# Kernel tuning notes

Hardware: AMD Instinct MI355X
Metric: run time of the kernel (lower is better)

## Reference

```python
import jax, jax.numpy as jnp
import numpy as np

N, D = 8192, 512


def _l2norm(x):
    return x / jnp.linalg.norm(x, axis=-1, keepdims=True)


def setup_inputs() -> dict:
    key = jax.random.key(0)
    k1, k2 = jax.random.split(key)
    image_features = _l2norm(jax.random.normal(k1, (N, D), dtype=jnp.float32))
    text_features = _l2norm(jax.random.normal(k2, (N, D), dtype=jnp.float32))
    logit_scale = jnp.asarray(100.0, dtype=jnp.float32)  # exp(4.6), standard CLIP temperature
    return {"image_features": image_features, "text_features": text_features, "logit_scale": logit_scale}


def reference(image_features, text_features, logit_scale):
    # logits_per_image = scale * img @ txt.T ; logits_per_text is its transpose (world_size=1)
    logits = logit_scale * (image_features @ text_features.T)  # [N, N]
    n = logits.shape[0]
    idx = jnp.arange(n)
    # CE with labels = arange(N): loss = -mean(diag(log_softmax(logits)))
    lse_row = jax.nn.logsumexp(logits, axis=1)  # for logits_per_image
    lse_col = jax.nn.logsumexp(logits, axis=0)  # for logits_per_text = logits.T
    diag = logits[idx, idx]
    loss_i = jnp.mean(lse_row - diag)
    loss_t = jnp.mean(lse_col - diag)
    contrastive_loss = (loss_i + loss_t) / 2
    return contrastive_loss
```

## Files before the change

kernel.cpp:

```cpp
#include <hip/hip_runtime.h>
#include <stdint.h>

#define N_ROWS 8192
#define DDIM   512

typedef __bf16 bf16_t;
typedef bf16_t bf16x8 __attribute__((ext_vector_type(8)));
typedef float  f32x4  __attribute__((ext_vector_type(4)));

#define MFMA16 __builtin_amdgcn_mfma_f32_16x16x32_bf16

__device__ inline uint16_t f2bf(float f) {
    uint32_t u = __float_as_uint(f);
    u += 0x7FFFu + ((u >> 16) & 1u);
    return (uint16_t)(u >> 16);
}

__global__ void convert_bf16(const float* __restrict__ a, const float* __restrict__ b,
                             uint16_t* __restrict__ abf, uint16_t* __restrict__ bbf) {
    const int quads = N_ROWS * DDIM / 4;
    const int stride = gridDim.x * blockDim.x;
    for (int i = blockIdx.x * blockDim.x + threadIdx.x; i < quads; i += stride) {
        float4 va = ((const float4*)a)[i];
        float4 vb = ((const float4*)b)[i];
        ushort4 ra, rb;
        ra.x = f2bf(va.x); ra.y = f2bf(va.y); ra.z = f2bf(va.z); ra.w = f2bf(va.w);
        rb.x = f2bf(vb.x); rb.y = f2bf(vb.y); rb.z = f2bf(vb.z); rb.w = f2bf(vb.w);
        ((ushort4*)abf)[i] = ra;
        ((ushort4*)bbf)[i] = rb;
    }
}

__device__ inline void stage16(const uint8_t* g, uint8_t* lds_wave_base) {
#if __has_builtin(__builtin_amdgcn_global_load_lds)
    __builtin_amdgcn_global_load_lds(
        (const __attribute__((address_space(1))) uint32_t*)g,
        (__attribute__((address_space(3))) uint32_t*)lds_wave_base, 16, 0, 0);
#else
    *(int4*)(lds_wave_base) = *(const int4*)g;
#endif
}

__global__ void __launch_bounds__(512, 2)
clip_gemm(const uint16_t* __restrict__ A, const uint16_t* __restrict__ B,
          const float* __restrict__ scale_p,
          float* __restrict__ rowsum, float* __restrict__ colsum,
          float* __restrict__ diag) {
    __shared__ __attribute__((aligned(16))) uint8_t sh[131072];

    const int t    = threadIdx.x;
    const int wave = t >> 6;
    const int lane = t & 63;
    const int wm   = wave >> 2;
    const int wn   = wave & 3;
    const int lr   = lane & 15;
    const int lg   = lane >> 4;
    const int l7   = lane & 7;

    const int orig = blockIdx.x;
    const int xcd  = orig & 7;
    const int idx  = orig >> 3;
    const int bm   = (xcd & 3) * 8  + (idx & 7);
    const int bn   = (xcd >> 2) * 16 + (idx >> 3);

    const float s     = *scale_p;
    const float shift = s - 64.0f;

    f32x4 acc[8][4];
#pragma unroll
    for (int i = 0; i < 8; ++i)
#pragma unroll
        for (int j = 0; j < 4; ++j)
#pragma unroll
            for (int r = 0; r < 4; ++r) acc[i][j][r] = 0.0f;

    const int g16 = (((t & 7) ^ ((t >> 3) & 7)) << 4);
    const uint8_t* srcA = (const uint8_t*)A + (size_t)(bm * 256 + (t >> 3)) * 1024 + g16;
    const uint8_t* srcB = (const uint8_t*)B + (size_t)(bn * 256 + (t >> 3)) * 1024 + g16;
    uint8_t* dA = sh + wave * 1024;
    uint8_t* dB = sh + 32768 + wave * 1024;

#define STAGE8(kt, bsel) do {                                                   \
        _Pragma("unroll")                                                       \
        for (int c = 0; c < 4; ++c) {                                           \
            stage16(srcA + (size_t)(kt) * 128 + (size_t)c * 65536,              \
                    dA + (bsel) * 65536 + c * 8192);                            \
            stage16(srcB + (size_t)(kt) * 128 + (size_t)c * 65536,              \
                    dB + (bsel) * 65536 + c * 8192);                            \
        }                                                                       \
    } while (0)

    const int x0   = ((lg) ^ l7) << 4;
    const int x1   = ((4 | lg) ^ l7) << 4;
    const int aRow = (wm * 128 + lr) * 128;
    const int bRow = 32768 + (wn * 64 + lr) * 128;

    bf16x8 aC[8], bC[4], aN[8], bN[4];

#define LOAD12(AF, BF, BASE, X) do {                                            \
        const uint8_t* _b = (BASE);                                             \
        _Pragma("unroll")                                                       \
        for (int i = 0; i < 8; ++i)                                             \
            AF[i] = *(const bf16x8*)(_b + aRow + i * 2048 + (X));               \
        _Pragma("unroll")                                                       \
        for (int j = 0; j < 4; ++j)                                             \
            BF[j] = *(const bf16x8*)(_b + bRow + j * 2048 + (X));               \
    } while (0)

#define MMA32(AF, BF) do {                                                      \
        _Pragma("unroll")                                                       \
        for (int i = 0; i < 8; ++i)                                             \
            _Pragma("unroll")                                                   \
            for (int j = 0; j < 4; ++j)                                         \
                acc[i][j] = MFMA16(AF[i], BF[j], acc[i][j], 0, 0, 0);           \
    } while (0)

    STAGE8(0, 0);
    STAGE8(1, 1);
    asm volatile("s_waitcnt vmcnt(8)" ::: "memory");
    __builtin_amdgcn_s_barrier();

    LOAD12(aC, bC, sh, x0);

    for (int tt = 0; tt < 8; ++tt) {
        const uint8_t* base  = sh + (tt & 1) * 65536;
        const uint8_t* obase = sh + ((tt + 1) & 1) * 65536;

        LOAD12(aN, bN, base, x1);
        __builtin_amdgcn_s_setprio(1);
        MMA32(aC, bC);
        __builtin_amdgcn_s_setprio(0);

        asm volatile("s_waitcnt vmcnt(0)" ::: "memory");
        __builtin_amdgcn_s_barrier();

        if (tt < 6) STAGE8(tt + 2, tt & 1);
        if (tt < 7) LOAD12(aC, bC, obase, x0);
        __builtin_amdgcn_s_setprio(1);
        MMA32(aN, bN);
        __builtin_amdgcn_s_setprio(0);
    }
#undef STAGE8
#undef LOAD12
#undef MMA32

    float cp[4] = {0.f, 0.f, 0.f, 0.f};
#pragma unroll
    for (int i = 0; i < 8; ++i) {
        float rp[4] = {0.f, 0.f, 0.f, 0.f};
#pragma unroll
        for (int j = 0; j < 4; ++j) {
#pragma unroll
            for (int r = 0; r < 4; ++r) {
                const float logit = s * acc[i][j][r];
                const float e = __expf(logit - shift);
                rp[r] += e;
                cp[j] += e;
                if (bm == bn) {
                    const int rr = wm * 128 + i * 16 + lg * 4 + r;
                    const int cc = wn * 64 + j * 16 + lr;
                    if (rr == cc) diag[bm * 256 + rr] = logit;
                }
            }
        }
#pragma unroll
        for (int r = 0; r < 4; ++r) {
            float v = rp[r];
            v += __shfl_xor(v, 1);
            v += __shfl_xor(v, 2);
            v += __shfl_xor(v, 4);
            v += __shfl_xor(v, 8);
            if (lr == 0)
                atomicAdd(&rowsum[bm * 256 + wm * 128 + i * 16 + lg * 4 + r], v);
        }
    }
#pragma unroll
    for (int j = 0; j < 4; ++j) {
        float v = cp[j];
        v += __shfl_xor(v, 16);
        v += __shfl_xor(v, 32);
        if (lg == 0)
            atomicAdd(&colsum[bn * 256 + wn * 64 + j * 16 + lr], v);
    }
}

__global__ void clip_finalize(const float* __restrict__ rowsum, const float* __restrict__ colsum,
                              const float* __restrict__ diag, const float* __restrict__ scale_p,
                              float* __restrict__ out) {
    __shared__ float red[4];
    const float s = *scale_p;
    const float shift = s - 64.0f;
    const int i = blockIdx.x * 256 + threadIdx.x;
    float acc = logf(rowsum[i]) + logf(colsum[i]) + 2.f * shift - 2.f * diag[i];
#pragma unroll
    for (int m = 1; m < 64; m <<= 1) acc += __shfl_xor(acc, m);
    const int wave = threadIdx.x >> 6;
    const int lane = threadIdx.x & 63;
    if (lane == 0) red[wave] = acc;
    __syncthreads();
    if (threadIdx.x == 0) {
        atomicAdd(out, (red[0] + red[1] + red[2] + red[3]) / (2.0f * N_ROWS));
    }
}

extern "C" void kernel_launch(void* const* d_in, const int* in_sizes, int n_in,
                              void* d_out, int out_size, void* d_ws, size_t ws_size,
                              hipStream_t stream) {
    const float* img     = (const float*)d_in[0];
    const float* txt     = (const float*)d_in[1];
    const float* scale_p = (const float*)d_in[2];

    uint8_t* ws = (uint8_t*)d_ws;
    uint16_t* Abf   = (uint16_t*)ws;
    uint16_t* Bbf   = (uint16_t*)(ws + (size_t)8 * 1024 * 1024);
    float*    rowsum = (float*)(ws + (size_t)16 * 1024 * 1024);
    float*    colsum = rowsum + N_ROWS;
    float*    diag   = colsum + N_ROWS;
    float*    out    = (float*)d_out;

    hipMemsetAsync(rowsum, 0, 2 * N_ROWS * sizeof(float), stream);
    hipMemsetAsync(out, 0, sizeof(float), stream);
    convert_bf16<<<1024, 256, 0, stream>>>(img, txt, Abf, Bbf);
    clip_gemm<<<1024, 512, 0, stream>>>(Abf, Bbf, scale_p, rowsum, colsum, diag);
    clip_finalize<<<32, 256, 0, stream>>>(rowsum, colsum, diag, scale_p, out);
}
```

Baseline: 105.0 us.

## Restructure GEMM main loop into four-phase quadrant pipeline with interleaved staging

Replaces the two-half K-step loop with a per-tile schedule split into four phases. Each phase computes one 4x2 quadrant of the accumulator tile, reads the next quadrant's LDS fragments, and issues a quarter of the next tile's global-to-LDS loads. Barriers bracket each MFMA block and vmcnt gates are finer-grained, so global loads, LDS reads and MFMAs overlap more evenly instead of stalling on a full vmcnt(0) once per half step. The cost is many more barriers per tile and a more fragile register-rotation scheme.

```diff
diff --git a/kernel.cpp b/kernel.cpp
--- a/kernel.cpp
+++ b/kernel.cpp
@@ -80,69 +80,104 @@
     uint8_t* dA = sh + wave * 1024;
     uint8_t* dB = sh + 32768 + wave * 1024;
 
-#define STAGE8(kt, bsel) do {                                                   \
-        _Pragma("unroll")                                                       \
-        for (int c = 0; c < 4; ++c) {                                           \
-            stage16(srcA + (size_t)(kt) * 128 + (size_t)c * 65536,              \
-                    dA + (bsel) * 65536 + c * 8192);                            \
-            stage16(srcB + (size_t)(kt) * 128 + (size_t)c * 65536,              \
-                    dB + (bsel) * 65536 + c * 8192);                            \
-        }                                                                       \
-    } while (0)
+#define STG_A(P, BS, c) stage16((P) + (size_t)(c) * 65536, dA + (BS) * 65536 + (c) * 8192)
+#define STG_B(P, BS, c) stage16((P) + (size_t)(c) * 65536, dB + (BS) * 65536 + (c) * 8192)
 
     const int x0   = ((lg) ^ l7) << 4;
     const int x1   = ((4 | lg) ^ l7) << 4;
     const int aRow = (wm * 128 + lr) * 128;
     const int bRow = 32768 + (wn * 64 + lr) * 128;
 
-    bf16x8 aC[8], bC[4], aN[8], bN[4];
-
-#define LOAD12(AF, BF, BASE, X) do {                                            \
-        const uint8_t* _b = (BASE);                                             \
-        _Pragma("unroll")                                                       \
-        for (int i = 0; i < 8; ++i)                                             \
-            AF[i] = *(const bf16x8*)(_b + aRow + i * 2048 + (X));               \
-        _Pragma("unroll")                                                       \
-        for (int j = 0; j < 4; ++j)                                             \
-            BF[j] = *(const bf16x8*)(_b + bRow + j * 2048 + (X));               \
-    } while (0)
-
-#define MMA32(AF, BF) do {                                                      \
-        _Pragma("unroll")                                                       \
-        for (int i = 0; i < 8; ++i)                                             \
-            _Pragma("unroll")                                                   \
-            for (int j = 0; j < 4; ++j)                                         \
-                acc[i][j] = MFMA16(AF[i], BF[j], acc[i][j], 0, 0, 0);           \
-    } while (0)
-
-    STAGE8(0, 0);
-    STAGE8(1, 1);
+    bf16x8 aA[2][4], aB[2][4], aC[2][4];
+    bf16x8 bA[2][2], bB[2][2];
+
+#define RD_AH(SET, BASE, IH) do {                                              \
+        const uint8_t* _p = (const uint8_t*)(BASE) + aRow + (IH) * 8192;       \
+        _Pragma("unroll")                                                      \
+        for (int _i = 0; _i < 4; ++_i) {                                       \
+            SET[0][_i] = *(const bf16x8*)(_p + _i * 2048 + x0);                \
+            SET[1][_i] = *(const bf16x8*)(_p + _i * 2048 + x1);                \
+        }                                                                      \
+    } while (0)
+
+#define RD_BH(SET, BASE, JH) do {                                              \
+        const uint8_t* _p = (const uint8_t*)(BASE) + bRow + (JH) * 4096;       \
+        _Pragma("unroll")                                                      \
+        for (int _j = 0; _j < 2; ++_j) {                                       \
+            SET[0][_j] = *(const bf16x8*)(_p + _j * 2048 + x0);                \
+            SET[1][_j] = *(const bf16x8*)(_p + _j * 2048 + x1);                \
+        }                                                                      \
+    } while (0)
+
+#define MMQ(IH, JH, AS, BS) do {                                               \
+        _Pragma("unroll")                                                      \
+        for (int _k = 0; _k < 2; ++_k)                                         \
+        _Pragma("unroll")                                                      \
+        for (int _i = 0; _i < 4; ++_i)                                         \
+        _Pragma("unroll")                                                      \
+        for (int _j = 0; _j < 2; ++_j)                                         \
+            acc[(IH) * 4 + _i][(JH) * 2 + _j] =                                \
+                MFMA16(AS[_k][_i], BS[_k][_j],                                 \
+                       acc[(IH) * 4 + _i][(JH) * 2 + _j], 0, 0, 0);            \
+    } while (0)
+
+#define GATE_VM4  asm volatile("s_waitcnt vmcnt(4)" ::: "memory")
+#define GATE_VM0  asm volatile("s_waitcnt vmcnt(0)" ::: "memory")
+#define GATE_NONE ((void)0)
+
+#define PH(RD, STG, GATE, IH, JH, AS, BS) do {                                 \
+        RD;                                                                    \
+        STG;                                                                   \
+        GATE;                                                                  \
+        __builtin_amdgcn_s_barrier();                                          \
+        __builtin_amdgcn_s_setprio(1);                                         \
+        MMQ(IH, JH, AS, BS);                                                   \
+        __builtin_amdgcn_s_setprio(0);                                         \
+        __builtin_amdgcn_s_barrier();                                          \
+    } while (0)
+
+#define TILE(BUF, OBUF, AP, AR, PSA, PSB, BS, NEXT, GATE)                      \
+    PH(RD_AH(aC, BUF, 1),                                                      \
+       do { if (PSA) { STG_A(PSA, BS, 0); STG_A(PSA, BS, 1); } } while (0),    \
+       GATE_NONE, 0, 0, AP, bA);                                               \
+    PH(RD_BH(bB, BUF, 1),                                                      \
+       do { if (PSA) { STG_A(PSA, BS, 2); STG_A(PSA, BS, 3); } } while (0),    \
+       GATE, 1, 0, aC, bA);                                                    \
+    PH(do { if (NEXT) RD_AH(AR, OBUF, 0); } while (0),                         \
+       do { if (PSB) { STG_B(PSB, BS, 0); STG_B(PSB, BS, 1); } } while (0),    \
+       GATE_NONE, 0, 1, AP, bB);                                               \
+    PH(do { if (NEXT) RD_BH(bA, OBUF, 0); } while (0),                         \
+       do { if (PSB) { STG_B(PSB, BS, 2); STG_B(PSB, BS, 3); } } while (0),    \
+       GATE_NONE, 1, 1, aC, bB)
+
+#pragma unroll
+    for (int c = 0; c < 4; ++c) { STG_A(srcA, 0, c); STG_B(srcB, 0, c); }
+#pragma unroll
+    for (int c = 0; c < 4; ++c) { STG_A(srcA + 128, 1, c); STG_B(srcB + 128, 1, c); }
     asm volatile("s_waitcnt vmcnt(8)" ::: "memory");
     __builtin_amdgcn_s_barrier();
-
-    LOAD12(aC, bC, sh, x0);
-
-    for (int tt = 0; tt < 8; ++tt) {
-        const uint8_t* base  = sh + (tt & 1) * 65536;
-        const uint8_t* obase = sh + ((tt + 1) & 1) * 65536;
-
-        LOAD12(aN, bN, base, x1);
-        __builtin_amdgcn_s_setprio(1);
-        MMA32(aC, bC);
-        __builtin_amdgcn_s_setprio(0);
-
-        asm volatile("s_waitcnt vmcnt(0)" ::: "memory");
-        __builtin_amdgcn_s_barrier();
-
-        if (tt < 6) STAGE8(tt + 2, tt & 1);
-        if (tt < 7) LOAD12(aC, bC, obase, x0);
-        __builtin_amdgcn_s_setprio(1);
-        MMA32(aN, bN);
-        __builtin_amdgcn_s_setprio(0);
-    }
-#undef STAGE8
-#undef LOAD12
-#undef MMA32
+    RD_AH(aA, sh, 0);
+    RD_BH(bA, sh, 0);
+
+    for (int p = 0; p < 3; ++p) {
+        const uint8_t* puA = srcA + (size_t)(2 * p + 2) * 128;
+        const uint8_t* puB = srcB + (size_t)(2 * p + 2) * 128;
+        TILE(sh,         sh + 65536, aA, aB, puA,       puB,       0, 1, GATE_VM4);
+        TILE(sh + 65536, sh,         aB, aA, puA + 128, puB + 128, 1, 1, GATE_VM4);
+    }
+    TILE(sh,         sh + 65536, aA, aB, (const uint8_t*)0, (const uint8_t*)0, 0, 1, GATE_VM0);
+    TILE(sh + 65536, sh,         aB, aA, (const uint8_t*)0, (const uint8_t*)0, 1, 0, GATE_NONE);
+
+#undef TILE
+#undef PH
+#undef GATE_NONE
+#undef GATE_VM0
+#undef GATE_VM4
+#undef MMQ
+#undef RD_BH
+#undef RD_AH
+#undef STG_B
+#undef STG_A
 
     float cp[4] = {0.f, 0.f, 0.f, 0.f};
 #pragma unroll
```

New measurement: 108.2 us. +3.1%, slower.

## Hand-schedule LDS reads with inline asm and deepen global-load pipelining

Applied to the files above, without the earlier changes.

Replaces compiler-generated LDS fragment loads with inline-asm ds_read_b128 using precomputed LDS offsets and immediate offsets. Adds explicit lgkmcnt waits and sched_barriers so fragment reads overlap the MFMA block. Global staging now waits only for the previous tile (vmcnt(8)) instead of draining all loads, which keeps one tile of global-to-LDS traffic in flight across iterations. The cost is an extra workgroup barrier per iteration, and the manual waits become a correctness risk if the counts are wrong.

```diff
diff --git a/kernel.cpp b/kernel.cpp
--- a/kernel.cpp
+++ b/kernel.cpp
@@ -7,6 +7,7 @@
 typedef __bf16 bf16_t;
 typedef bf16_t bf16x8 __attribute__((ext_vector_type(8)));
 typedef float  f32x4  __attribute__((ext_vector_type(4)));
+typedef __attribute__((address_space(3))) uint8_t lds_t;
 
 #define MFMA16 __builtin_amdgcn_mfma_f32_16x16x32_bf16
 
@@ -95,54 +96,78 @@
     const int aRow = (wm * 128 + lr) * 128;
     const int bRow = 32768 + (wn * 64 + lr) * 128;
 
-    bf16x8 aC[8], bC[4], aN[8], bN[4];
-
-#define LOAD12(AF, BF, BASE, X) do {                                            \
-        const uint8_t* _b = (BASE);                                             \
-        _Pragma("unroll")                                                       \
-        for (int i = 0; i < 8; ++i)                                             \
-            AF[i] = *(const bf16x8*)(_b + aRow + i * 2048 + (X));               \
-        _Pragma("unroll")                                                       \
-        for (int j = 0; j < 4; ++j)                                             \
-            BF[j] = *(const bf16x8*)(_b + bRow + j * 2048 + (X));               \
+    const uint32_t shOff = (uint32_t)(uintptr_t)(lds_t*)sh;
+    const uint32_t aX0 = shOff + (uint32_t)(aRow + x0);
+    const uint32_t aX1 = shOff + (uint32_t)(aRow + x1);
+    const uint32_t bX0 = shOff + (uint32_t)(bRow + x0);
+    const uint32_t bX1 = shOff + (uint32_t)(bRow + x1);
+
+#define DSR(dst, addr, off) \
+    asm volatile("ds_read_b128 %0, %1 offset:%2" : "=&v"(dst) : "v"(addr), "i"(off))
+
+#define RD12(AF, BF, AADDR, BADDR) do {                                         \
+        const uint32_t _aa = (AADDR), _bb = (BADDR);                            \
+        DSR(AF[0], _aa, 0);     DSR(AF[1], _aa, 2048);                          \
+        DSR(AF[2], _aa, 4096);  DSR(AF[3], _aa, 6144);                          \
+        DSR(AF[4], _aa, 8192);  DSR(AF[5], _aa, 10240);                         \
+        DSR(AF[6], _aa, 12288); DSR(AF[7], _aa, 14336);                         \
+        DSR(BF[0], _bb, 0);     DSR(BF[1], _bb, 2048);                          \
+        DSR(BF[2], _bb, 4096);  DSR(BF[3], _bb, 6144);                          \
     } while (0)
 
 #define MMA32(AF, BF) do {                                                      \
+        __builtin_amdgcn_s_setprio(1);                                          \
         _Pragma("unroll")                                                       \
         for (int i = 0; i < 8; ++i)                                             \
             _Pragma("unroll")                                                   \
             for (int j = 0; j < 4; ++j)                                         \
                 acc[i][j] = MFMA16(AF[i], BF[j], acc[i][j], 0, 0, 0);           \
+        __builtin_amdgcn_s_setprio(0);                                          \
     } while (0)
+
+#define WLG12() asm volatile("s_waitcnt lgkmcnt(12)" ::: "memory")
+#define WLG0()  asm volatile("s_waitcnt lgkmcnt(0)"  ::: "memory")
+#define WVM8()  asm volatile("s_waitcnt vmcnt(8)"    ::: "memory")
+#define WVM0()  asm volatile("s_waitcnt vmcnt(0)"    ::: "memory")
+#define SB0()   __builtin_amdgcn_sched_barrier(0)
+
+    bf16x8 aC[8], bC[4], aN[8], bN[4];
 
     STAGE8(0, 0);
     STAGE8(1, 1);
-    asm volatile("s_waitcnt vmcnt(8)" ::: "memory");
+    WVM8();
     __builtin_amdgcn_s_barrier();
-
-    LOAD12(aC, bC, sh, x0);
+    RD12(aC, bC, aX0, bX0);
 
     for (int tt = 0; tt < 8; ++tt) {
-        const uint8_t* base  = sh + (tt & 1) * 65536;
-        const uint8_t* obase = sh + ((tt + 1) & 1) * 65536;
-
-        LOAD12(aN, bN, base, x1);
-        __builtin_amdgcn_s_setprio(1);
+        const uint32_t cb = (uint32_t)((tt & 1) << 16);
+        const uint32_t nb = (uint32_t)(((tt + 1) & 1) << 16);
+
+        RD12(aN, bN, aX1 + cb, bX1 + cb);
+        WLG12();
+        SB0();
         MMA32(aC, bC);
-        __builtin_amdgcn_s_setprio(0);
-
-        asm volatile("s_waitcnt vmcnt(0)" ::: "memory");
+        WLG0();
+        SB0();
         __builtin_amdgcn_s_barrier();
 
-        if (tt < 6) STAGE8(tt + 2, tt & 1);
-        if (tt < 7) LOAD12(aC, bC, obase, x0);
-        __builtin_amdgcn_s_setprio(1);
+        if (tt < 6)      { STAGE8(tt + 2, tt & 1); WVM8(); }
+        else if (tt == 6) { WVM0(); }
+        __builtin_amdgcn_s_barrier();
+
+        if (tt < 7) RD12(aC, bC, aX0 + nb, bX0 + nb);
+        SB0();
         MMA32(aN, bN);
-        __builtin_amdgcn_s_setprio(0);
     }
 #undef STAGE8
-#undef LOAD12
+#undef RD12
 #undef MMA32
+#undef DSR
+#undef WLG12
+#undef WLG0
+#undef WVM8
+#undef WVM0
+#undef SB0
 
     float cp[4] = {0.f, 0.f, 0.f, 0.f};
 #pragma unroll
```

New measurement: 108.0 us. +2.9%, slower.

## Keep full-K A tile resident in LDS and stream B fragments from global

Applied to the files above, without the earlier changes.

Replaces the 256x256 double-buffered LDS GEMM tile with a 128x256 tile per block. The block's whole 128x512 A slab (128 KB) is loaded into LDS once, and each wave reads its B fragments straight from global memory into registers, prefetching one K-step ahead. The grid doubles to 2048 blocks with a simpler block mapping. Row and column partial sums are first reduced in LDS, then written with one global atomic per element. The change removes repeated LDS staging and barriers in the K loop, but it depends on global and L2 latency for B, and the full 128 KB of LDS may limit how many blocks fit per CU.

```diff
diff --git a/kernel.cpp b/kernel.cpp
--- a/kernel.cpp
+++ b/kernel.cpp
@@ -51,8 +51,6 @@
     const int t    = threadIdx.x;
     const int wave = t >> 6;
     const int lane = t & 63;
-    const int wm   = wave >> 2;
-    const int wn   = wave & 3;
     const int lr   = lane & 15;
     const int lg   = lane >> 4;
     const int l7   = lane & 7;
@@ -60,107 +58,95 @@
     const int orig = blockIdx.x;
     const int xcd  = orig & 7;
     const int idx  = orig >> 3;
-    const int bm   = (xcd & 3) * 8  + (idx & 7);
-    const int bn   = (xcd >> 2) * 16 + (idx >> 3);
+    const int bm   = xcd * 8 + (idx & 7);
+    const int bn   = idx >> 3;
 
     const float s     = *scale_p;
     const float shift = s - 64.0f;
 
-    f32x4 acc[8][4];
+    f32x4 acc[8][2];
 #pragma unroll
     for (int i = 0; i < 8; ++i)
 #pragma unroll
-        for (int j = 0; j < 4; ++j)
+        for (int j = 0; j < 2; ++j)
 #pragma unroll
             for (int r = 0; r < 4; ++r) acc[i][j][r] = 0.0f;
 
-    const int g16 = (((t & 7) ^ ((t >> 3) & 7)) << 4);
-    const uint8_t* srcA = (const uint8_t*)A + (size_t)(bm * 256 + (t >> 3)) * 1024 + g16;
-    const uint8_t* srcB = (const uint8_t*)B + (size_t)(bn * 256 + (t >> 3)) * 1024 + g16;
-    uint8_t* dA = sh + wave * 1024;
-    uint8_t* dB = sh + 32768 + wave * 1024;
-
-#define STAGE8(kt, bsel) do {                                                   \
+    {
+        const uint8_t* srcA = (const uint8_t*)A
+            + (size_t)(bm * 128 + wave) * 1024 + ((lane ^ wave) << 4);
+        uint8_t* dA = sh + wave * 1024;
+#pragma unroll
+        for (int c = 0; c < 16; ++c)
+            stage16(srcA + (size_t)c * 8192, dA + c * 8192);
+    }
+    asm volatile("s_waitcnt vmcnt(0)" ::: "memory");
+    __builtin_amdgcn_s_barrier();
+
+    const uint8_t* Bp0 = (const uint8_t*)B
+        + (size_t)(bn * 256 + wave * 32 + lr) * 1024;
+    const uint8_t* Bp1 = Bp0 + 16 * 1024;
+
+    bf16x8 af[2][8], bfr[2][2];
+
+#define LOADA(D, KS) do {                                                       \
+        const int _sl = ((((KS) << 2) | lg) ^ l7) << 4;                         \
+        const uint8_t* _p = sh + lr * 1024 + _sl;                               \
         _Pragma("unroll")                                                       \
-        for (int c = 0; c < 4; ++c) {                                           \
-            stage16(srcA + (size_t)(kt) * 128 + (size_t)c * 65536,              \
-                    dA + (bsel) * 65536 + c * 8192);                            \
-            stage16(srcB + (size_t)(kt) * 128 + (size_t)c * 65536,              \
-                    dB + (bsel) * 65536 + c * 8192);                            \
-        }                                                                       \
+        for (int _i = 0; _i < 8; ++_i)                                          \
+            af[D][_i] = *(const bf16x8*)(_p + _i * 16384);                      \
     } while (0)
 
-    const int x0   = ((lg) ^ l7) << 4;
-    const int x1   = ((4 | lg) ^ l7) << 4;
-    const int aRow = (wm * 128 + lr) * 128;
-    const int bRow = 32768 + (wn * 64 + lr) * 128;
-
-    bf16x8 aC[8], bC[4], aN[8], bN[4];
-
-#define LOAD12(AF, BF, BASE, X) do {                                            \
-        const uint8_t* _b = (BASE);                                             \
+#define LOADB(D, KS) do {                                                       \
+        const int _ko = (KS) * 64 + lg * 16;                                    \
+        bfr[D][0] = *(const bf16x8*)(Bp0 + _ko);                                \
+        bfr[D][1] = *(const bf16x8*)(Bp1 + _ko);                                \
+    } while (0)
+
+#define MMA(D) do {                                                             \
+        __builtin_amdgcn_s_setprio(1);                                          \
         _Pragma("unroll")                                                       \
-        for (int i = 0; i < 8; ++i)                                             \
-            AF[i] = *(const bf16x8*)(_b + aRow + i * 2048 + (X));               \
-        _Pragma("unroll")                                                       \
-        for (int j = 0; j < 4; ++j)                                             \
-            BF[j] = *(const bf16x8*)(_b + bRow + j * 2048 + (X));               \
+        for (int _i = 0; _i < 8; ++_i)                                          \
+            _Pragma("unroll")                                                   \
+            for (int _j = 0; _j < 2; ++_j)                                      \
+                acc[_i][_j] = MFMA16(af[D][_i], bfr[D][_j], acc[_i][_j], 0, 0, 0); \
+        __builtin_amdgcn_s_setprio(0);                                          \
     } while (0)
 
-#define MMA32(AF, BF) do {                                                      \
-        _Pragma("unroll")                                                       \
-        for (int i = 0; i < 8; ++i)                                             \
-            _Pragma("unroll")                                                   \
-            for (int j = 0; j < 4; ++j)                                         \
-                acc[i][j] = MFMA16(AF[i], BF[j], acc[i][j], 0, 0, 0);           \
-    } while (0)
-
-    STAGE8(0, 0);
-    STAGE8(1, 1);
-    asm volatile("s_waitcnt vmcnt(8)" ::: "memory");
-    __builtin_amdgcn_s_barrier();
-
-    LOAD12(aC, bC, sh, x0);
-
-    for (int tt = 0; tt < 8; ++tt) {
-        const uint8_t* base  = sh + (tt & 1) * 65536;
-        const uint8_t* obase = sh + ((tt + 1) & 1) * 65536;
-
-        LOAD12(aN, bN, base, x1);
-        __builtin_amdgcn_s_setprio(1);
-        MMA32(aC, bC);
-        __builtin_amdgcn_s_setprio(0);
-
-        asm volatile("s_waitcnt vmcnt(0)" ::: "memory");
-        __builtin_amdgcn_s_barrier();
-
-        if (tt < 6) STAGE8(tt + 2, tt & 1);
-        if (tt < 7) LOAD12(aC, bC, obase, x0);
-        __builtin_amdgcn_s_setprio(1);
-        MMA32(aN, bN);
-        __builtin_amdgcn_s_setprio(0);
-    }
-#undef STAGE8
-#undef LOAD12
-#undef MMA32
-
-    float cp[4] = {0.f, 0.f, 0.f, 0.f};
+    LOADA(0, 0);
+    LOADB(0, 0);
+#pragma unroll
+    for (int ks = 0; ks < 16; ++ks) {
+        const int cur = ks & 1, nxt = cur ^ 1;
+        if (ks < 15) { LOADA(nxt, ks + 1); LOADB(nxt, ks + 1); }
+        MMA(cur);
+    }
+#undef LOADA
+#undef LOADB
+#undef MMA
+
+    __syncthreads();
+    float* rs = (float*)sh;
+    float* cs = rs + 128;
+    if (t < 128)      rs[t] = 0.f;
+    else if (t < 384) cs[t - 128] = 0.f;
+    __syncthreads();
+
+    float cp[2] = {0.f, 0.f};
 #pragma unroll
     for (int i = 0; i < 8; ++i) {
         float rp[4] = {0.f, 0.f, 0.f, 0.f};
 #pragma unroll
-        for (int j = 0; j < 4; ++j) {
+        for (int j = 0; j < 2; ++j) {
 #pragma unroll
             for (int r = 0; r < 4; ++r) {
                 const float logit = s * acc[i][j][r];
                 const float e = __expf(logit - shift);
                 rp[r] += e;
                 cp[j] += e;
-                if (bm == bn) {
-                    const int rr = wm * 128 + i * 16 + lg * 4 + r;
-                    const int cc = wn * 64 + j * 16 + lr;
-                    if (rr == cc) diag[bm * 256 + rr] = logit;
-                }
+                const int rowg = bm * 128 + i * 16 + lg * 4 + r;
+                const int colg = bn * 256 + wave * 32 + j * 16 + lr;
+                if (rowg == colg) diag[rowg] = logit;
             }
         }
 #pragma unroll
@@ -170,18 +156,19 @@
             v += __shfl_xor(v, 2);
             v += __shfl_xor(v, 4);
             v += __shfl_xor(v, 8);
-            if (lr == 0)
-                atomicAdd(&rowsum[bm * 256 + wm * 128 + i * 16 + lg * 4 + r], v);
+            if (lr == 0) atomicAdd(&rs[i * 16 + lg * 4 + r], v);
         }
     }
 #pragma unroll
-    for (int j = 0; j < 4; ++j) {
+    for (int j = 0; j < 2; ++j) {
         float v = cp[j];
         v += __shfl_xor(v, 16);
         v += __shfl_xor(v, 32);
-        if (lg == 0)
-            atomicAdd(&colsum[bn * 256 + wn * 64 + j * 16 + lr], v);
-    }
+        if (lg == 0) cs[wave * 32 + j * 16 + lr] = v;
+    }
+    __syncthreads();
+    if (t < 128)      atomicAdd(&rowsum[bm * 128 + t], rs[t]);
+    else if (t < 384) atomicAdd(&colsum[bn * 256 + (t - 128)], cs[t - 128]);
 }
 
 __global__ void clip_finalize(const float* __restrict__ rowsum, const float* __restrict__ colsum,
@@ -221,6 +208,6 @@
     hipMemsetAsync(rowsum, 0, 2 * N_ROWS * sizeof(float), stream);
     hipMemsetAsync(out, 0, sizeof(float), stream);
     convert_bf16<<<1024, 256, 0, stream>>>(img, txt, Abf, Bbf);
-    clip_gemm<<<1024, 512, 0, stream>>>(Abf, Bbf, scale_p, rowsum, colsum, diag);
+    clip_gemm<<<2048, 512, 0, stream>>>(Abf, Bbf, scale_p, rowsum, colsum, diag);
     clip_finalize<<<32, 256, 0, stream>>>(rowsum, colsum, diag, scale_p, out);
 }
```

Result: slower. 149.3 us (+42.2%).
